# Kernel tuning notes

Measured on AMD Instinct MI355X. Metric: run time of the kernel, lower is better.

The kernel has to match this reference:

```python
import jax, jax.numpy as jnp
import numpy as np

EPS = 1e-5
B, C, N_A, N_B, P, M = 128, 32, 12, 12, 8192, 2


def _bn(x, gamma, beta, mean, var):
    # x: (B, C, P); per-channel inference batch norm
    scale = gamma * jax.lax.rsqrt(var + EPS)
    return x * scale[None, :, None] + (beta - mean * scale)[None, :, None]


def setup_inputs() -> dict:
    key = jax.random.key(0)
    ks = jax.random.split(key, 12)
    return {
        "feat_a": jax.random.normal(ks[0], (B, C, N_A), jnp.float32),
        "feat_b": jax.random.normal(ks[1], (B, C, N_B), jnp.float32),
        "assign_a": jax.random.randint(ks[2], (P, M), 0, N_A, jnp.int32),
        "assign_b": jax.random.randint(ks[3], (P, M), 0, N_B, jnp.int32),
        "bn1_gamma": jax.random.uniform(ks[4], (C,), jnp.float32, 0.5, 1.5),
        "bn1_beta": jax.random.normal(ks[5], (C,), jnp.float32) * 0.1,
        "bn1_mean": jax.random.normal(ks[6], (C,), jnp.float32) * 0.1,
        "bn1_var": jax.random.uniform(ks[7], (C,), jnp.float32, 0.5, 1.5),
        "conv_w": jax.random.normal(ks[8], (C, C), jnp.float32) / np.sqrt(C),
        "bn2_gamma": jax.random.uniform(ks[9], (C,), jnp.float32, 0.5, 1.5),
        "bn2_beta": jax.random.normal(ks[10], (C,), jnp.float32) * 0.1,
        "bn2_mean": jax.random.normal(ks[11], (C,), jnp.float32) * 0.1,
        "bn2_var": jnp.ones((C,), jnp.float32),
    }


def reference(feat_a, feat_b, assign_a, assign_b,
              bn1_gamma, bn1_beta, bn1_mean, bn1_var,
              conv_w, bn2_gamma, bn2_beta, bn2_mean, bn2_var):
    # Gather product features via permutation indices: (B, C, P, M)
    ga = feat_a[:, :, assign_a].max(axis=-1)  # max over constituents -> (B, C, P)
    gb = feat_b[:, :, assign_b].max(axis=-1)
    agg = jnp.maximum(ga, gb)                 # 'max' aggregation across products
    x = _bn(agg, bn1_gamma, bn1_beta, bn1_mean, bn1_var)
    x = jnp.einsum('oc,bcp->bop', conv_w, x)  # 1x1 Conv1d, no bias
    x = _bn(x, bn2_gamma, bn2_beta, bn2_mean, bn2_var)
    return jax.nn.relu(x)
```

## Files before the change

### kernel.cpp

```cpp
#include <hip/hip_runtime.h>


#define EPS 1e-5f
constexpr int B  = 128;
constexpr int C  = 32;
constexpr int NA = 12;
constexpr int PP = 8192;
constexpr int PT = 256;
constexpr int FS = 36;
constexpr int XS = 40;

typedef short bfv8  __attribute__((ext_vector_type(8)));
typedef float f32x4 __attribute__((ext_vector_type(4)));

__device__ __forceinline__ ushort f2bf(float f) {
    uint u = __float_as_uint(f);
    u += 0x7fffu + ((u >> 16) & 1u);
    return (ushort)(u >> 16);
}
__device__ __forceinline__ float bf2f(ushort h) {
    return __uint_as_float(((uint)h) << 16);
}
__device__ __forceinline__ uint pk(ushort lo, ushort hi) {
    return (uint)lo | ((uint)hi << 16);
}

__global__ __launch_bounds__(256) void fold_kernel(
    const float* __restrict__ conv_w,
    const float* __restrict__ g1, const float* __restrict__ b1,
    const float* __restrict__ m1, const float* __restrict__ v1,
    const float* __restrict__ g2, const float* __restrict__ b2,
    const float* __restrict__ m2, const float* __restrict__ v2,
    ushort* __restrict__ afh, ushort* __restrict__ afl,
    float* __restrict__ bpp)
{
    __shared__ float s1[C], t1[C], s2[C], t2[C], w2[C * C];
    int tid = threadIdx.x;
    if (tid < C) {
        float s = g1[tid] * rsqrtf(v1[tid] + EPS);
        s1[tid] = s;
        t1[tid] = b1[tid] - m1[tid] * s;
        float ss = g2[tid] * rsqrtf(v2[tid] + EPS);
        s2[tid] = ss;
        t2[tid] = b2[tid] - m2[tid] * ss;
    }
    __syncthreads();
    for (int i = tid; i < C * C; i += 256) {
        int o = i >> 5, c = i & 31;
        w2[i] = conv_w[i] * s1[c] * s2[o];
    }
    if (tid < C) {
        float acc = 0.f;
        for (int c = 0; c < C; ++c) acc += conv_w[tid * C + c] * t1[c];
        bpp[tid] = acc * s2[tid] + t2[tid];
    }
    __syncthreads();
#pragma unroll
    for (int e = tid * 4; e < tid * 4 + 4; ++e) {
        int t = e >> 9, l = (e >> 3) & 63, j = e & 7;
        int m = (l & 15) + 16 * t;
        int k = (l >> 4) * 8 + j;
        float w = w2[m * C + k];
        ushort h = f2bf(w);
        afh[e] = h;
        afl[e] = f2bf(w - bf2f(h));
    }
}

__global__ __launch_bounds__(256) void main_kernel(
    const float* __restrict__ feat_a, const float* __restrict__ feat_b,
    const int*   __restrict__ assign_a, const int* __restrict__ assign_b,
    const ushort* __restrict__ afh, const ushort* __restrict__ afl,
    const float* __restrict__ bpp,
    float* __restrict__ out)
{
    __shared__ __align__(16) float  fa[NA * FS];
    __shared__ __align__(16) float  fb[NA * FS];
    __shared__ __align__(16) ushort xh[PT * XS];
    __shared__ __align__(16) ushort xl[PT * XS];

    const int tid  = threadIdx.x;
    const int lane = tid & 63;
    const int b    = blockIdx.x >> 5;
    const int p0   = (blockIdx.x & 31) * PT;
    const int q    = lane >> 4;
    const int n    = lane & 15;

    bfv8 ah0 = *(const bfv8*)(afh + lane * 8);
    bfv8 ah1 = *(const bfv8*)(afh + 512 + lane * 8);
    bfv8 al0 = *(const bfv8*)(afl + lane * 8);
    bfv8 al1 = *(const bfv8*)(afl + 512 + lane * 8);
    float bias0[4], bias1[4];
#pragma unroll
    for (int r = 0; r < 4; ++r) {
        bias0[r] = bpp[q * 4 + r];
        bias1[r] = bpp[16 + q * 4 + r];
    }

    for (int i = tid; i < C * NA; i += 256) {
        int c = i / NA, nn = i - c * NA;
        fa[nn * FS + c] = feat_a[b * C * NA + i];
        fb[nn * FS + c] = feat_b[b * C * NA + i];
    }
    __syncthreads();

    {
        const int p = p0 + tid;
        const int2 ia = ((const int2*)assign_a)[p];
        const int2 ib = ((const int2*)assign_b)[p];
        const float* a0 = &fa[ia.x * FS];
        const float* a1 = &fa[ia.y * FS];
        const float* c0 = &fb[ib.x * FS];
        const float* c1 = &fb[ib.y * FS];

        float x[C];
#pragma unroll
        for (int cc = 0; cc < C; cc += 4) {
            float4 va0 = *(const float4*)(a0 + cc);
            float4 va1 = *(const float4*)(a1 + cc);
            float4 vb0 = *(const float4*)(c0 + cc);
            float4 vb1 = *(const float4*)(c1 + cc);
            x[cc + 0] = fmaxf(fmaxf(va0.x, va1.x), fmaxf(vb0.x, vb1.x));
            x[cc + 1] = fmaxf(fmaxf(va0.y, va1.y), fmaxf(vb0.y, vb1.y));
            x[cc + 2] = fmaxf(fmaxf(va0.z, va1.z), fmaxf(vb0.z, vb1.z));
            x[cc + 3] = fmaxf(fmaxf(va0.w, va1.w), fmaxf(vb0.w, vb1.w));
        }

        ushort* rowh = &xh[tid * XS];
        ushort* rowl = &xl[tid * XS];
#pragma unroll
        for (int c = 0; c < C; c += 8) {
            ushort h[8], l[8];
#pragma unroll
            for (int j = 0; j < 8; ++j) {
                float v = x[c + j];
                h[j] = f2bf(v);
                l[j] = f2bf(v - bf2f(h[j]));
            }
            uint4 vh = make_uint4(pk(h[0], h[1]), pk(h[2], h[3]),
                                  pk(h[4], h[5]), pk(h[6], h[7]));
            uint4 vl = make_uint4(pk(l[0], l[1]), pk(l[2], l[3]),
                                  pk(l[4], l[5]), pk(l[6], l[7]));
            *(uint4*)(rowh + c) = vh;
            *(uint4*)(rowl + c) = vl;
        }
    }
    __syncthreads();

    const int wave = tid >> 6;
    const f32x4 zero = {0.f, 0.f, 0.f, 0.f};
    float* outb = out + b * C * PP + p0;
#pragma unroll
    for (int ch = 0; ch < 4; ++ch) {
        const int base = (wave * 4 + ch) * 16;
        const bfv8 bh = *(const bfv8*)&xh[(base + n) * XS + q * 8];
        const bfv8 bl = *(const bfv8*)&xl[(base + n) * XS + q * 8];

        f32x4 d0 = __builtin_amdgcn_mfma_f32_16x16x32_bf16(ah0, bh, zero, 0, 0, 0);
        d0       = __builtin_amdgcn_mfma_f32_16x16x32_bf16(ah0, bl, d0,   0, 0, 0);
        d0       = __builtin_amdgcn_mfma_f32_16x16x32_bf16(al0, bh, d0,   0, 0, 0);
        f32x4 d1 = __builtin_amdgcn_mfma_f32_16x16x32_bf16(ah1, bh, zero, 0, 0, 0);
        d1       = __builtin_amdgcn_mfma_f32_16x16x32_bf16(ah1, bl, d1,   0, 0, 0);
        d1       = __builtin_amdgcn_mfma_f32_16x16x32_bf16(al1, bh, d1,   0, 0, 0);

        float* op = outb + base + n;
#pragma unroll
        for (int r = 0; r < 4; ++r) {
            op[(q * 4 + r) * PP]      = fmaxf(d0[r] + bias0[r], 0.f);
            op[(16 + q * 4 + r) * PP] = fmaxf(d1[r] + bias1[r], 0.f);
        }
    }
}

extern "C" void kernel_launch(void* const* d_in, const int* in_sizes, int n_in,
                              void* d_out, int out_size, void* d_ws, size_t ws_size,
                              hipStream_t stream) {
    const float* feat_a   = (const float*)d_in[0];
    const float* feat_b   = (const float*)d_in[1];
    const int*   assign_a = (const int*)  d_in[2];
    const int*   assign_b = (const int*)  d_in[3];
    const float* g1 = (const float*)d_in[4];
    const float* b1 = (const float*)d_in[5];
    const float* m1 = (const float*)d_in[6];
    const float* v1 = (const float*)d_in[7];
    const float* cw = (const float*)d_in[8];
    const float* g2 = (const float*)d_in[9];
    const float* b2 = (const float*)d_in[10];
    const float* m2 = (const float*)d_in[11];
    const float* v2 = (const float*)d_in[12];

    float* out = (float*)d_out;
    ushort* afh = (ushort*)d_ws;
    ushort* afl = (ushort*)((char*)d_ws + 2048);
    float*  bpp = (float*)((char*)d_ws + 4096);

    fold_kernel<<<1, 256, 0, stream>>>(cw, g1, b1, m1, v1, g2, b2, m2, v2,
                                       afh, afl, bpp);
    main_kernel<<<B * (PP / PT), 256, 0, stream>>>(feat_a, feat_b,
                                                   assign_a, assign_b,
                                                   afh, afl, bpp, out);
}
```

Measured before the change: 174.5 us.

## Fuse BN/weight fold into main kernel, drop activation low split, swizzle LDS

Removes the separate single-block fold kernel. Every block now recomputes the folded BN scales, the conv weights and the bias in shared memory and splits the weights into bf16 hi/lo in registers, which saves one launch and the dependency between the two kernels. Activations are stored only as bf16 hi, so two of the six MFMAs and the xl buffer are dropped. This lowers the accuracy of the activation operand. A rotation swizzle is added to the xh stores and loads to reduce LDS bank conflicts.

```diff
diff --git a/kernel.cpp b/kernel.cpp
--- a/kernel.cpp
+++ b/kernel.cpp
@@ -2,13 +2,14 @@
 
 
 #define EPS 1e-5f
-constexpr int B  = 128;
-constexpr int C  = 32;
-constexpr int NA = 12;
-constexpr int PP = 8192;
-constexpr int PT = 256;
-constexpr int FS = 36;
-constexpr int XS = 40;
+constexpr int B   = 128;
+constexpr int C   = 32;
+constexpr int NA  = 12;
+constexpr int PP  = 8192;
+constexpr int PT  = 256;
+constexpr int FS  = 36;
+constexpr int XS  = 40;
+constexpr int W2S = 36;
 
 typedef short bfv8  __attribute__((ext_vector_type(8)));
 typedef float f32x4 __attribute__((ext_vector_type(4)));
@@ -25,59 +26,21 @@
     return (uint)lo | ((uint)hi << 16);
 }
 
-__global__ __launch_bounds__(256) void fold_kernel(
+__global__ __launch_bounds__(256) void main_kernel(
+    const float* __restrict__ feat_a, const float* __restrict__ feat_b,
+    const int*   __restrict__ assign_a, const int* __restrict__ assign_b,
     const float* __restrict__ conv_w,
     const float* __restrict__ g1, const float* __restrict__ b1,
     const float* __restrict__ m1, const float* __restrict__ v1,
     const float* __restrict__ g2, const float* __restrict__ b2,
     const float* __restrict__ m2, const float* __restrict__ v2,
-    ushort* __restrict__ afh, ushort* __restrict__ afl,
-    float* __restrict__ bpp)
-{
-    __shared__ float s1[C], t1[C], s2[C], t2[C], w2[C * C];
-    int tid = threadIdx.x;
-    if (tid < C) {
-        float s = g1[tid] * rsqrtf(v1[tid] + EPS);
-        s1[tid] = s;
-        t1[tid] = b1[tid] - m1[tid] * s;
-        float ss = g2[tid] * rsqrtf(v2[tid] + EPS);
-        s2[tid] = ss;
-        t2[tid] = b2[tid] - m2[tid] * ss;
-    }
-    __syncthreads();
-    for (int i = tid; i < C * C; i += 256) {
-        int o = i >> 5, c = i & 31;
-        w2[i] = conv_w[i] * s1[c] * s2[o];
-    }
-    if (tid < C) {
-        float acc = 0.f;
-        for (int c = 0; c < C; ++c) acc += conv_w[tid * C + c] * t1[c];
-        bpp[tid] = acc * s2[tid] + t2[tid];
-    }
-    __syncthreads();
-#pragma unroll
-    for (int e = tid * 4; e < tid * 4 + 4; ++e) {
-        int t = e >> 9, l = (e >> 3) & 63, j = e & 7;
-        int m = (l & 15) + 16 * t;
-        int k = (l >> 4) * 8 + j;
-        float w = w2[m * C + k];
-        ushort h = f2bf(w);
-        afh[e] = h;
-        afl[e] = f2bf(w - bf2f(h));
-    }
-}
-
-__global__ __launch_bounds__(256) void main_kernel(
-    const float* __restrict__ feat_a, const float* __restrict__ feat_b,
-    const int*   __restrict__ assign_a, const int* __restrict__ assign_b,
-    const ushort* __restrict__ afh, const ushort* __restrict__ afl,
-    const float* __restrict__ bpp,
     float* __restrict__ out)
 {
+    __shared__ float s1[C], t1[C], s2v[C], bsh[C];
+    __shared__ __align__(16) float  w2[C * W2S];
     __shared__ __align__(16) float  fa[NA * FS];
     __shared__ __align__(16) float  fb[NA * FS];
     __shared__ __align__(16) ushort xh[PT * XS];
-    __shared__ __align__(16) ushort xl[PT * XS];
 
     const int tid  = threadIdx.x;
     const int lane = tid & 63;
@@ -86,23 +49,55 @@
     const int q    = lane >> 4;
     const int n    = lane & 15;
 
-    bfv8 ah0 = *(const bfv8*)(afh + lane * 8);
-    bfv8 ah1 = *(const bfv8*)(afh + 512 + lane * 8);
-    bfv8 al0 = *(const bfv8*)(afl + lane * 8);
-    bfv8 al1 = *(const bfv8*)(afl + 512 + lane * 8);
-    float bias0[4], bias1[4];
-#pragma unroll
-    for (int r = 0; r < 4; ++r) {
-        bias0[r] = bpp[q * 4 + r];
-        bias1[r] = bpp[16 + q * 4 + r];
+    if (tid < C) {
+        float s = g1[tid] * rsqrtf(v1[tid] + EPS);
+        s1[tid]  = s;
+        t1[tid]  = b1[tid] - m1[tid] * s;
+        s2v[tid] = g2[tid] * rsqrtf(v2[tid] + EPS);
     }
-
     for (int i = tid; i < C * NA; i += 256) {
         int c = i / NA, nn = i - c * NA;
         fa[nn * FS + c] = feat_a[b * C * NA + i];
         fb[nn * FS + c] = feat_b[b * C * NA + i];
     }
     __syncthreads();
+
+    for (int i = tid; i < C * C; i += 256) {
+        int o = i >> 5, c = i & 31;
+        w2[o * W2S + c] = conv_w[i] * s1[c] * s2v[o];
+    }
+    if (tid < C) {
+        float acc = 0.f;
+        for (int c = 0; c < C; ++c) acc += conv_w[tid * C + c] * t1[c];
+        bsh[tid] = acc * s2v[tid] + (b2[tid] - m2[tid] * s2v[tid]);
+    }
+    __syncthreads();
+
+    bfv8 ah0, al0, ah1, al1;
+    {
+        float wv0[8], wv1[8];
+        const float* r0 = &w2[(lane & 15) * W2S + q * 8];
+        const float* r1 = &w2[((lane & 15) + 16) * W2S + q * 8];
+        *(float4*)&wv0[0] = *(const float4*)(r0);
+        *(float4*)&wv0[4] = *(const float4*)(r0 + 4);
+        *(float4*)&wv1[0] = *(const float4*)(r1);
+        *(float4*)&wv1[4] = *(const float4*)(r1 + 4);
+#pragma unroll
+        for (int j = 0; j < 8; ++j) {
+            ushort h0 = f2bf(wv0[j]);
+            ah0[j] = (short)h0;
+            al0[j] = (short)f2bf(wv0[j] - bf2f(h0));
+            ushort h1 = f2bf(wv1[j]);
+            ah1[j] = (short)h1;
+            al1[j] = (short)f2bf(wv1[j] - bf2f(h1));
+        }
+    }
+    float bias0[4], bias1[4];
+#pragma unroll
+    for (int r = 0; r < 4; ++r) {
+        bias0[r] = bsh[q * 4 + r];
+        bias1[r] = bsh[16 + q * 4 + r];
+    }
 
     {
         const int p = p0 + tid;
@@ -127,22 +122,16 @@
         }
 
         ushort* rowh = &xh[tid * XS];
-        ushort* rowl = &xl[tid * XS];
+        const int rot = (tid + (tid >> 3)) & 3;
 #pragma unroll
-        for (int c = 0; c < C; c += 8) {
-            ushort h[8], l[8];
+        for (int g = 0; g < 4; ++g) {
+            const int c = g * 8;
+            ushort h[8];
 #pragma unroll
-            for (int j = 0; j < 8; ++j) {
-                float v = x[c + j];
-                h[j] = f2bf(v);
-                l[j] = f2bf(v - bf2f(h[j]));
-            }
+            for (int j = 0; j < 8; ++j) h[j] = f2bf(x[c + j]);
             uint4 vh = make_uint4(pk(h[0], h[1]), pk(h[2], h[3]),
                                   pk(h[4], h[5]), pk(h[6], h[7]));
-            uint4 vl = make_uint4(pk(l[0], l[1]), pk(l[2], l[3]),
-                                  pk(l[4], l[5]), pk(l[6], l[7]));
-            *(uint4*)(rowh + c) = vh;
-            *(uint4*)(rowl + c) = vl;
+            *(uint4*)(rowh + ((g + rot) & 3) * 8) = vh;
         }
     }
     __syncthreads();
@@ -153,21 +142,20 @@
 #pragma unroll
     for (int ch = 0; ch < 4; ++ch) {
         const int base = (wave * 4 + ch) * 16;
-        const bfv8 bh = *(const bfv8*)&xh[(base + n) * XS + q * 8];
-        const bfv8 bl = *(const bfv8*)&xl[(base + n) * XS + q * 8];
+        const int r    = base + n;
+        const int slot = (q + r + (r >> 3)) & 3;
+        const bfv8 bh  = *(const bfv8*)&xh[r * XS + slot * 8];
 
         f32x4 d0 = __builtin_amdgcn_mfma_f32_16x16x32_bf16(ah0, bh, zero, 0, 0, 0);
-        d0       = __builtin_amdgcn_mfma_f32_16x16x32_bf16(ah0, bl, d0,   0, 0, 0);
         d0       = __builtin_amdgcn_mfma_f32_16x16x32_bf16(al0, bh, d0,   0, 0, 0);
         f32x4 d1 = __builtin_amdgcn_mfma_f32_16x16x32_bf16(ah1, bh, zero, 0, 0, 0);
-        d1       = __builtin_amdgcn_mfma_f32_16x16x32_bf16(ah1, bl, d1,   0, 0, 0);
         d1       = __builtin_amdgcn_mfma_f32_16x16x32_bf16(al1, bh, d1,   0, 0, 0);
 
         float* op = outb + base + n;
 #pragma unroll
-        for (int r = 0; r < 4; ++r) {
-            op[(q * 4 + r) * PP]      = fmaxf(d0[r] + bias0[r], 0.f);
-            op[(16 + q * 4 + r) * PP] = fmaxf(d1[r] + bias1[r], 0.f);
+        for (int rr = 0; rr < 4; ++rr) {
+            op[(q * 4 + rr) * PP]      = fmaxf(d0[rr] + bias0[rr], 0.f);
+            op[(16 + q * 4 + rr) * PP] = fmaxf(d1[rr] + bias1[rr], 0.f);
         }
     }
 }
@@ -190,13 +178,9 @@
     const float* v2 = (const float*)d_in[12];
 
     float* out = (float*)d_out;
-    ushort* afh = (ushort*)d_ws;
-    ushort* afl = (ushort*)((char*)d_ws + 2048);
-    float*  bpp = (float*)((char*)d_ws + 4096);
+    (void)d_ws; (void)ws_size;
 
-    fold_kernel<<<1, 256, 0, stream>>>(cw, g1, b1, m1, v1, g2, b2, m2, v2,
-                                       afh, afl, bpp);
-    main_kernel<<<B * (PP / PT), 256, 0, stream>>>(feat_a, feat_b,
-                                                   assign_a, assign_b,
-                                                   afh, afl, bpp, out);
+    main_kernel<<<B * (PP / PT), 256, 0, stream>>>(
+        feat_a, feat_b, assign_a, assign_b, cw,
+        g1, b1, m1, v1, g2, b2, m2, v2, out);
 }
```

After: 171.0 us. -2.0%, faster.
